# Kernel tuning notes

Hardware: AMD Instinct MI355X
Metric: run time of the kernel (lower is better)

The kernel has to match this reference:

```python
import jax, jax.numpy as jnp
import numpy as np

NUM_Q = 500000
NUM_E = 250000
DIM = 256
HEADS = 4
NEG_SLOPE = 0.01
EPS = 1e-16


def setup_inputs() -> dict:
    key = jax.random.key(0)
    k1, k2, k3, k4, k5 = jax.random.split(key, 5)
    x_q = jax.random.normal(k1, (NUM_Q, DIM), dtype=jnp.float32)
    x_edge = jax.random.normal(k2, (NUM_E, DIM), dtype=jnp.float32)
    edge_ids = jax.random.randint(k3, (NUM_Q,), 0, NUM_E, dtype=jnp.int64)
    # learned params: w_q (input_dim, output_dim), attention weight (H, 2*dim/H)
    w_q = jax.random.normal(k4, (DIM, DIM), dtype=jnp.float32) / np.sqrt(DIM)
    weight = jax.random.normal(k5, (HEADS, 2 * DIM // HEADS), dtype=jnp.float32) / np.sqrt(2 * DIM // HEADS)
    return {"x_q": x_q, "x_edge": x_edge, "w_q": w_q, "weight": weight, "edge_ids": edge_ids}


def reference(x_q, x_edge, w_q, weight, edge_ids):
    nq = x_q.shape[0]
    ne = x_edge.shape[0]
    h = weight.shape[0]
    # project qualifier pairs: (nq, dim) -> (nq, H, d_head)
    xq = (x_q @ w_q).reshape(nq, h, -1)
    # gather edge reps per qualifier pair: (nq, H, d_head)
    xe = x_edge[edge_ids].reshape(nq, h, -1)
    # per-head attention logits: eh
    alpha = jnp.einsum('ehd,hd->eh', jnp.concatenate([xe, xq], axis=-1), weight)
    alpha = jax.nn.leaky_relu(alpha, NEG_SLOPE)
    # segment softmax grouped by edge_ids (numerically stable)
    seg_max = jax.ops.segment_max(alpha, edge_ids, num_segments=ne)
    seg_max = jnp.where(jnp.isfinite(seg_max), seg_max, 0.0)  # empty segments
    ex = jnp.exp(alpha - seg_max[edge_ids])
    seg_sum = jax.ops.segment_sum(ex, edge_ids, num_segments=ne)
    alpha = ex / (seg_sum[edge_ids] + EPS)
    # weight qualifier reps and scatter-add to edges
    xq = (alpha[..., None] * xq).reshape(nq, -1)
    return jax.ops.segment_sum(xq, edge_ids, num_segments=ne)
```

## Files before the change

kernel.cpp:

```cpp
#include <hip/hip_runtime.h>
#include <hip/hip_bf16.h>

#define DIM 256
#define HEADS 4
#define NEG_SLOPE 0.01f

typedef unsigned short u16;
typedef __attribute__((ext_vector_type(8))) short short8;
typedef __attribute__((ext_vector_type(4))) float f32x4;

__device__ __forceinline__ u16 f2bf(float f) {
    unsigned u = __float_as_uint(f);
    unsigned r = (u + 0x7fffu + ((u >> 16) & 1u)) >> 16;
    return (u16)r;
}
__device__ __forceinline__ unsigned cvt2(float a, float b) {
    __hip_bfloat162 h = __float22bfloat162_rn(make_float2(a, b));
    unsigned u;
    __builtin_memcpy(&u, &h, 4);
    return u;
}

__global__ __launch_bounds__(256) void prepb_kernel(const float* __restrict__ B,
                                                    u16* __restrict__ BThi) {
    int k = blockIdx.x;
    int n = threadIdx.x;
    BThi[n * 256 + k] = f2bf(B[k * 256 + n]);
}

__global__ __launch_bounds__(256) void prepwg_kernel(const float* __restrict__ wq,
                                                     const float* __restrict__ weight,
                                                     float* __restrict__ wg) {
    int k = threadIdx.x;
#pragma unroll
    for (int h = 0; h < 4; ++h) {
        float s = 0.f;
        for (int d = 0; d < 64; ++d)
            s = fmaf(wq[k * 256 + h * 64 + d], weight[h * 128 + 64 + d], s);
        wg[k * 4 + h] = s;
    }
}

__global__ __launch_bounds__(256) void beta_kernel(const float* __restrict__ xe,
                                                   const float* __restrict__ weight,
                                                   float* __restrict__ beta, int NE) {
    int wid = blockIdx.x * 4 + (threadIdx.x >> 6);
    if (wid >= NE) return;
    int lane = threadIdx.x & 63;
    int h = lane >> 4;
    float4 v = *reinterpret_cast<const float4*>(xe + (size_t)wid * DIM + lane * 4);
    float4 w = *reinterpret_cast<const float4*>(weight + h * 128 + (lane & 15) * 4);
    float p = v.x * w.x + v.y * w.y + v.z * w.z + v.w * w.w;
    p += __shfl_xor(p, 1);
    p += __shfl_xor(p, 2);
    p += __shfl_xor(p, 4);
    p += __shfl_xor(p, 8);
    if ((lane & 15) == 0) beta[(size_t)wid * 4 + h] = p;
}

__global__ __launch_bounds__(256) void gamma_kernel(const float* __restrict__ xq,
                                                    const float* __restrict__ wg,
                                                    const float* __restrict__ beta,
                                                    const int* __restrict__ eids,
                                                    float* __restrict__ exv,
                                                    float* __restrict__ segsum,
                                                    unsigned* __restrict__ counts, int NQ) {
    int e = blockIdx.x * 4 + (threadIdx.x >> 6);
    if (e >= NQ) return;
    int lane = threadIdx.x & 63;
    float4 x = *reinterpret_cast<const float4*>(xq + (size_t)e * DIM + lane * 4);
    float4 p = make_float4(0.f, 0.f, 0.f, 0.f);
    const float xs[4] = {x.x, x.y, x.z, x.w};
#pragma unroll
    for (int i = 0; i < 4; ++i) {
        float4 w = *reinterpret_cast<const float4*>(wg + (lane * 4 + i) * 4);
        p.x = fmaf(xs[i], w.x, p.x);
        p.y = fmaf(xs[i], w.y, p.y);
        p.z = fmaf(xs[i], w.z, p.z);
        p.w = fmaf(xs[i], w.w, p.w);
    }
#pragma unroll
    for (int d = 1; d < 64; d <<= 1) {
        p.x += __shfl_xor(p.x, d);
        p.y += __shfl_xor(p.y, d);
        p.z += __shfl_xor(p.z, d);
        p.w += __shfl_xor(p.w, d);
    }
    if (lane == 0) {
        int j = eids[e];
        float4 b = *reinterpret_cast<const float4*>(beta + (size_t)j * 4);
        float l[4] = {b.x + p.x, b.y + p.y, b.z + p.z, b.w + p.w};
        float ex[4];
#pragma unroll
        for (int h = 0; h < 4; ++h) {
            l[h] = l[h] > 0.f ? l[h] : NEG_SLOPE * l[h];
            ex[h] = __expf(l[h]);
        }
        *reinterpret_cast<float4*>(exv + (size_t)e * 4) = make_float4(ex[0], ex[1], ex[2], ex[3]);
#pragma unroll
        for (int h = 0; h < 4; ++h) atomicAdd(&segsum[(size_t)j * 4 + h], ex[h]);
        atomicAdd(&counts[j], 1u);
    }
}

__global__ __launch_bounds__(256) void scan1_kernel(const unsigned* __restrict__ counts,
                                                    unsigned* __restrict__ offs,
                                                    unsigned* __restrict__ blocksums, int NE) {
    __shared__ unsigned s[256];
    int t = threadIdx.x;
    int base = blockIdx.x * 1024 + t * 4;
    unsigned v[4], sum = 0;
#pragma unroll
    for (int i = 0; i < 4; ++i) {
        v[i] = (base + i < NE) ? counts[base + i] : 0u;
        sum += v[i];
    }
    s[t] = sum;
    __syncthreads();
    for (int off = 1; off < 256; off <<= 1) {
        unsigned y = (t >= off) ? s[t - off] : 0u;
        __syncthreads();
        s[t] += y;
        __syncthreads();
    }
    unsigned excl = s[t] - sum;
#pragma unroll
    for (int i = 0; i < 4; ++i) {
        if (base + i < NE) offs[base + i] = excl;
        excl += v[i];
    }
    if (t == 255) blocksums[blockIdx.x] = s[255];
}

__global__ __launch_bounds__(256) void scan2_kernel(unsigned* __restrict__ blocksums, int NB) {
    __shared__ unsigned s[256];
    int t = threadIdx.x;
    unsigned v = (t < NB) ? blocksums[t] : 0u;
    s[t] = v;
    __syncthreads();
    for (int off = 1; off < 256; off <<= 1) {
        unsigned y = (t >= off) ? s[t - off] : 0u;
        __syncthreads();
        s[t] += y;
        __syncthreads();
    }
    if (t < NB) blocksums[t] = s[t] - v;
}

__global__ __launch_bounds__(256) void scan3_kernel(unsigned* __restrict__ offs,
                                                    const unsigned* __restrict__ blocksums,
                                                    unsigned* __restrict__ cursor, int NE) {
    int t = threadIdx.x;
    int base = blockIdx.x * 1024 + t * 4;
    unsigned add = blocksums[blockIdx.x];
#pragma unroll
    for (int i = 0; i < 4; ++i) {
        if (base + i < NE) {
            unsigned o = offs[base + i] + add;
            offs[base + i] = o;
            cursor[base + i] = o;
        }
    }
}

__global__ __launch_bounds__(256) void fill_kernel(const int* __restrict__ eids,
                                                   unsigned* __restrict__ cursor,
                                                   int* __restrict__ qlist, int NQ) {
    int e = blockIdx.x * blockDim.x + threadIdx.x;
    if (e >= NQ) return;
    int j = eids[e];
    unsigned pos = atomicAdd(&cursor[j], 1u);
    qlist[pos] = e;
}

__global__ __launch_bounds__(256, 3) void aggmm_kernel(const float* __restrict__ xq,
                                                       const u16* __restrict__ BThi,
                                                       const float* __restrict__ exv,
                                                       const float* __restrict__ segsum,
                                                       const unsigned* __restrict__ offs,
                                                       const unsigned* __restrict__ counts,
                                                       const int* __restrict__ qlist,
                                                       float* __restrict__ out, int NE) {
    __shared__ u16 agg_s[64 * 256];

    const int t = threadIdx.x;
    const int e_loc = t >> 4;
    const int tc = t & 15;
    const long j = (long)blockIdx.x * 16 + e_loc;
    const bool ok_e = j < NE;

    f32x4 acc[4][4];
#pragma unroll
    for (int h = 0; h < 4; ++h)
#pragma unroll
        for (int i = 0; i < 4; ++i) acc[h][i] = (f32x4){0.f, 0.f, 0.f, 0.f};

    if (ok_e) {
        unsigned beg = offs[j];
        unsigned n = counts[j];
        float4 ss = *reinterpret_cast<const float4*>(segsum + (size_t)j * 4);
        float inv[4] = {1.f / (ss.x + 1e-16f), 1.f / (ss.y + 1e-16f),
                        1.f / (ss.z + 1e-16f), 1.f / (ss.w + 1e-16f)};
        for (unsigned i = 0; i < n; ++i) {
            int q = qlist[beg + i];
            float4 e4 = *reinterpret_cast<const float4*>(exv + (size_t)q * 4);
            float w[4] = {e4.x * inv[0], e4.y * inv[1], e4.z * inv[2], e4.w * inv[3]};
            const float* xr = xq + (size_t)q * DIM + tc * 16;
            float4 xv[4];
#pragma unroll
            for (int c = 0; c < 4; ++c) xv[c] = *reinterpret_cast<const float4*>(xr + c * 4);
#pragma unroll
            for (int h = 0; h < 4; ++h)
#pragma unroll
                for (int c = 0; c < 4; ++c) {
                    acc[h][c].x = fmaf(w[h], xv[c].x, acc[h][c].x);
                    acc[h][c].y = fmaf(w[h], xv[c].y, acc[h][c].y);
                    acc[h][c].z = fmaf(w[h], xv[c].z, acc[h][c].z);
                    acc[h][c].w = fmaf(w[h], xv[c].w, acc[h][c].w);
                }
        }
    }

#pragma unroll
    for (int h = 0; h < 4; ++h) {
        int row = e_loc * 4 + h;
#pragma unroll
        for (int c = 0; c < 2; ++c) {
            uint4 wv;
            wv.x = cvt2(acc[h][c * 2].x, acc[h][c * 2].y);
            wv.y = cvt2(acc[h][c * 2].z, acc[h][c * 2].w);
            wv.z = cvt2(acc[h][c * 2 + 1].x, acc[h][c * 2 + 1].y);
            wv.w = cvt2(acc[h][c * 2 + 1].z, acc[h][c * 2 + 1].w);
            int chunk = (tc * 2 + c) ^ (row & 7);
            *reinterpret_cast<uint4*>(&agg_s[row * 256 + chunk * 8]) = wv;
        }
    }
    __syncthreads();

    const int wave = t >> 6;
    const int lane = t & 63;
    const int lr = lane & 15;
    const int kg = lane >> 4;
    const int arow = lr * 4 + wave;
    const u16* brows[4];
#pragma unroll
    for (int n = 0; n < 4; ++n)
        brows[n] = BThi + (wave * 64 + n * 16 + lr) * 256 + kg * 8;

    f32x4 cc[4];
#pragma unroll
    for (int n = 0; n < 4; ++n) cc[n] = (f32x4){0.f, 0.f, 0.f, 0.f};

#pragma unroll
    for (int k0 = 0; k0 < DIM; k0 += 32) {
        int chunk = ((k0 >> 3) + kg) ^ (arow & 7);
        short8 ah = *reinterpret_cast<const short8*>(&agg_s[arow * 256 + chunk * 8]);
#pragma unroll
        for (int n = 0; n < 4; ++n) {
            short8 bh = *reinterpret_cast<const short8*>(brows[n] + k0);
            cc[n] = __builtin_amdgcn_mfma_f32_16x16x32_bf16(ah, bh, cc[n], 0, 0, 0);
        }
    }

#pragma unroll
    for (int r = 0; r < 4; ++r) {
        long jj = (long)blockIdx.x * 16 + kg * 4 + r;
        if (jj < NE) {
            float* orow = out + jj * DIM + wave * 64 + lr;
#pragma unroll
            for (int n = 0; n < 4; ++n) orow[n * 16] = cc[n][r];
        }
    }
}

extern "C" void kernel_launch(void* const* d_in, const int* in_sizes, int n_in,
                              void* d_out, int out_size, void* d_ws, size_t ws_size,
                              hipStream_t stream) {
    (void)n_in; (void)out_size; (void)ws_size;
    const float* x_q    = (const float*)d_in[0];
    const float* x_edge = (const float*)d_in[1];
    const float* w_q    = (const float*)d_in[2];
    const float* weight = (const float*)d_in[3];
    const int*   eids   = (const int*)d_in[4];
    const int NQ = in_sizes[0] / DIM;
    const int NE = in_sizes[1] / DIM;
    float* out = (float*)d_out;

    float*    exv       = (float*)d_ws;
    float*    beta      = exv + (size_t)NQ * 4;
    float*    segsum    = beta + (size_t)NE * 4;
    unsigned* counts    = (unsigned*)(segsum + (size_t)NE * 4);
    unsigned* offs      = counts + NE;
    unsigned* cursor    = offs + NE;
    int*      qlist     = (int*)(cursor + NE);
    unsigned* blocksums = (unsigned*)(qlist + NQ);
    u16*      BThi      = (u16*)(blocksums + 256);
    float*    wg        = (float*)(BThi + 256 * 256);

    const int NB = (NE + 1023) / 1024;

    hipMemsetAsync(segsum, 0, (size_t)NE * 4 * sizeof(float), stream);
    hipMemsetAsync(counts, 0, (size_t)NE * sizeof(unsigned), stream);

    prepb_kernel<<<256, 256, 0, stream>>>(w_q, BThi);
    prepwg_kernel<<<1, 256, 0, stream>>>(w_q, weight, wg);
    beta_kernel<<<(NE + 3) / 4, 256, 0, stream>>>(x_edge, weight, beta, NE);
    gamma_kernel<<<(NQ + 3) / 4, 256, 0, stream>>>(x_q, wg, beta, eids, exv, segsum, counts, NQ);
    scan1_kernel<<<NB, 256, 0, stream>>>(counts, offs, blocksums, NE);
    scan2_kernel<<<1, 256, 0, stream>>>(blocksums, NB);
    scan3_kernel<<<NB, 256, 0, stream>>>(offs, blocksums, cursor, NE);
    fill_kernel<<<(NQ + 255) / 256, 256, 0, stream>>>(eids, cursor, qlist, NQ);
    aggmm_kernel<<<(NE + 15) / 16, 256, 0, stream>>>(x_q, BThi, exv, segsum, offs, counts,
                                                     qlist, out, NE);
}
```

Before: 702.3 us.

## Assign one wave per edge in aggregation and split MFMA across 8 waves

The aggregation kernel now runs 512 threads per block. Each wave handles two edges in turn, and each lane loads one float4 of the gathered x_q row, so a whole 1 KB row is read coalesced per qualifier. Before, 16 threads per edge each loaded 64 bytes. The MFMA stage is split across 8 waves (head × column half), so each wave computes two 16x16 output tiles instead of four. This aims to improve memory coalescing and latency hiding on the gather-heavy phase. The cost is that edges are processed serially within a wave, which brings divergence from uneven segment lengths.

```diff
diff --git a/kernel.cpp b/kernel.cpp
--- a/kernel.cpp
+++ b/kernel.cpp
@@ -173,7 +173,7 @@
     qlist[pos] = e;
 }
 
-__global__ __launch_bounds__(256, 3) void aggmm_kernel(const float* __restrict__ xq,
+__global__ __launch_bounds__(512, 4) void aggmm_kernel(const float* __restrict__ xq,
                                                        const u16* __restrict__ BThi,
                                                        const float* __restrict__ exv,
                                                        const float* __restrict__ segsum,
@@ -184,91 +184,73 @@
     __shared__ u16 agg_s[64 * 256];
 
     const int t = threadIdx.x;
-    const int e_loc = t >> 4;
-    const int tc = t & 15;
-    const long j = (long)blockIdx.x * 16 + e_loc;
-    const bool ok_e = j < NE;
-
-    f32x4 acc[4][4];
-#pragma unroll
-    for (int h = 0; h < 4; ++h)
-#pragma unroll
-        for (int i = 0; i < 4; ++i) acc[h][i] = (f32x4){0.f, 0.f, 0.f, 0.f};
-
-    if (ok_e) {
-        unsigned beg = offs[j];
-        unsigned n = counts[j];
-        float4 ss = *reinterpret_cast<const float4*>(segsum + (size_t)j * 4);
-        float inv[4] = {1.f / (ss.x + 1e-16f), 1.f / (ss.y + 1e-16f),
-                        1.f / (ss.z + 1e-16f), 1.f / (ss.w + 1e-16f)};
-        for (unsigned i = 0; i < n; ++i) {
-            int q = qlist[beg + i];
-            float4 e4 = *reinterpret_cast<const float4*>(exv + (size_t)q * 4);
-            float w[4] = {e4.x * inv[0], e4.y * inv[1], e4.z * inv[2], e4.w * inv[3]};
-            const float* xr = xq + (size_t)q * DIM + tc * 16;
-            float4 xv[4];
-#pragma unroll
-            for (int c = 0; c < 4; ++c) xv[c] = *reinterpret_cast<const float4*>(xr + c * 4);
-#pragma unroll
-            for (int h = 0; h < 4; ++h)
-#pragma unroll
-                for (int c = 0; c < 4; ++c) {
-                    acc[h][c].x = fmaf(w[h], xv[c].x, acc[h][c].x);
-                    acc[h][c].y = fmaf(w[h], xv[c].y, acc[h][c].y);
-                    acc[h][c].z = fmaf(w[h], xv[c].z, acc[h][c].z);
-                    acc[h][c].w = fmaf(w[h], xv[c].w, acc[h][c].w);
-                }
-        }
-    }
-
-#pragma unroll
-    for (int h = 0; h < 4; ++h) {
-        int row = e_loc * 4 + h;
-#pragma unroll
-        for (int c = 0; c < 2; ++c) {
-            uint4 wv;
-            wv.x = cvt2(acc[h][c * 2].x, acc[h][c * 2].y);
-            wv.y = cvt2(acc[h][c * 2].z, acc[h][c * 2].w);
-            wv.z = cvt2(acc[h][c * 2 + 1].x, acc[h][c * 2 + 1].y);
-            wv.w = cvt2(acc[h][c * 2 + 1].z, acc[h][c * 2 + 1].w);
-            int chunk = (tc * 2 + c) ^ (row & 7);
-            *reinterpret_cast<uint4*>(&agg_s[row * 256 + chunk * 8]) = wv;
+    const int w = t >> 6;
+    const int lane = t & 63;
+
+    for (int e2 = 0; e2 < 2; ++e2) {
+        const int e_loc = w * 2 + e2;
+        const long j = (long)blockIdx.x * 16 + e_loc;
+        f32x4 a0 = (f32x4){0.f, 0.f, 0.f, 0.f};
+        f32x4 a1 = a0, a2 = a0, a3 = a0;
+        if (j < NE) {
+            const unsigned beg = offs[j];
+            const unsigned n = counts[j];
+            float4 ss = *reinterpret_cast<const float4*>(segsum + (size_t)j * 4);
+            const float inv0 = 1.f / (ss.x + 1e-16f);
+            const float inv1 = 1.f / (ss.y + 1e-16f);
+            const float inv2 = 1.f / (ss.z + 1e-16f);
+            const float inv3 = 1.f / (ss.w + 1e-16f);
+            const float* xcol = xq + lane * 4;
+#pragma unroll 2
+            for (unsigned i = 0; i < n; ++i) {
+                int q = qlist[beg + i];
+                float4 e4 = *reinterpret_cast<const float4*>(exv + (size_t)q * 4);
+                float4 xv = *reinterpret_cast<const float4*>(xcol + (size_t)q * DIM);
+                f32x4 xvv = {xv.x, xv.y, xv.z, xv.w};
+                a0 += (e4.x * inv0) * xvv;
+                a1 += (e4.y * inv1) * xvv;
+                a2 += (e4.z * inv2) * xvv;
+                a3 += (e4.w * inv3) * xvv;
+            }
+        }
+        const int halfsel = (lane & 1) * 4;
+        f32x4 accs[4] = {a0, a1, a2, a3};
+#pragma unroll
+        for (int h = 0; h < 4; ++h) {
+            int row = e_loc * 4 + h;
+            int chunk = (lane >> 1) ^ (row & 7);
+            uint2 wv = make_uint2(cvt2(accs[h][0], accs[h][1]), cvt2(accs[h][2], accs[h][3]));
+            *reinterpret_cast<uint2*>(&agg_s[row * 256 + chunk * 8 + halfsel]) = wv;
         }
     }
     __syncthreads();
 
-    const int wave = t >> 6;
-    const int lane = t & 63;
+    const int h = w >> 1;
+    const int gp = w & 1;
     const int lr = lane & 15;
     const int kg = lane >> 4;
-    const int arow = lr * 4 + wave;
-    const u16* brows[4];
-#pragma unroll
-    for (int n = 0; n < 4; ++n)
-        brows[n] = BThi + (wave * 64 + n * 16 + lr) * 256 + kg * 8;
-
-    f32x4 cc[4];
-#pragma unroll
-    for (int n = 0; n < 4; ++n) cc[n] = (f32x4){0.f, 0.f, 0.f, 0.f};
-
-#pragma unroll
-    for (int k0 = 0; k0 < DIM; k0 += 32) {
-        int chunk = ((k0 >> 3) + kg) ^ (arow & 7);
-        short8 ah = *reinterpret_cast<const short8*>(&agg_s[arow * 256 + chunk * 8]);
-#pragma unroll
-        for (int n = 0; n < 4; ++n) {
-            short8 bh = *reinterpret_cast<const short8*>(brows[n] + k0);
-            cc[n] = __builtin_amdgcn_mfma_f32_16x16x32_bf16(ah, bh, cc[n], 0, 0, 0);
-        }
-    }
-
+    const int rowA = lr * 4 + h;
+    const u16* bptr0 = BThi + (h * 64 + gp * 32 + lr) * 256 + kg * 8;
+    const u16* bptr1 = bptr0 + 16 * 256;
+
+    f32x4 cc0 = (f32x4){0.f, 0.f, 0.f, 0.f};
+    f32x4 cc1 = cc0;
+#pragma unroll
+    for (int s = 0; s < 8; ++s) {
+        int phys = (s * 4 + kg) ^ (rowA & 7);
+        short8 ah = *reinterpret_cast<const short8*>(&agg_s[rowA * 256 + phys * 8]);
+        short8 b0 = *reinterpret_cast<const short8*>(bptr0 + s * 32);
+        short8 b1 = *reinterpret_cast<const short8*>(bptr1 + s * 32);
+        cc0 = __builtin_amdgcn_mfma_f32_16x16x32_bf16(ah, b0, cc0, 0, 0, 0);
+        cc1 = __builtin_amdgcn_mfma_f32_16x16x32_bf16(ah, b1, cc1, 0, 0, 0);
+    }
 #pragma unroll
     for (int r = 0; r < 4; ++r) {
         long jj = (long)blockIdx.x * 16 + kg * 4 + r;
         if (jj < NE) {
-            float* orow = out + jj * DIM + wave * 64 + lr;
-#pragma unroll
-            for (int n = 0; n < 4; ++n) orow[n * 16] = cc[n][r];
+            float* orow = out + jj * DIM + h * 64 + gp * 32 + lr;
+            orow[0]  = cc0[r];
+            orow[16] = cc1[r];
         }
     }
 }
@@ -310,6 +292,6 @@
     scan2_kernel<<<1, 256, 0, stream>>>(blocksums, NB);
     scan3_kernel<<<NB, 256, 0, stream>>>(offs, blocksums, cursor, NE);
     fill_kernel<<<(NQ + 255) / 256, 256, 0, stream>>>(eids, cursor, qlist, NQ);
-    aggmm_kernel<<<(NE + 15) / 16, 256, 0, stream>>>(x_q, BThi, exv, segsum, offs, counts,
+    aggmm_kernel<<<(NE + 15) / 16, 512, 0, stream>>>(x_q, BThi, exv, segsum, offs, counts,
                                                      qlist, out, NE);
 }
```

Result: faster. 681.8 us (-2.9%).
